# Performance work log

Hardware: AMD Instinct MI355X
Metric: run time of the kernel (lower is better)

## Reference

```python
import jax, jax.numpy as jnp
import numpy as np

TAU = 0.5

def setup_inputs() -> dict:
    key = jax.random.key(0)
    ks = jax.random.split(key, 8)
    B_Nq, B_Ns, C, H, W = 16, 16, 512, 32, 32
    f_q = jax.random.normal(ks[0], (B_Nq, C, H, W), dtype=jnp.float32)
    f_s = jax.random.normal(ks[1], (B_Ns, C, H, W), dtype=jnp.float32)
    # depthwise 1x1 convs with groups=dim, bias=False -> per-channel scalar weights [C]
    w_cca_q = jax.random.normal(ks[2], (C,), dtype=jnp.float32)
    w_cca_k = jax.random.normal(ks[3], (C,), dtype=jnp.float32)
    w_cca_v = jax.random.normal(ks[4], (C,), dtype=jnp.float32)
    w_sca_q = jax.random.normal(ks[5], (C,), dtype=jnp.float32)
    w_sca_k = jax.random.normal(ks[6], (C,), dtype=jnp.float32)
    lam = jnp.float32(0.1)
    return {"f_q": f_q, "f_s": f_s, "w_cca_q": w_cca_q, "w_cca_k": w_cca_k,
            "w_cca_v": w_cca_v, "w_sca_q": w_sca_q, "w_sca_k": w_sca_k, "lam": lam}

def _dw(x, w):
    # depthwise 1x1 conv, no bias == per-channel scale; x: [B,C,H,W], w: [C]
    return x * w[None, :, None, None]

def reference(f_q, f_s, w_cca_q, w_cca_k, w_cca_v, w_sca_q, w_sca_k, lam):
    B_Nq, C, H, W = f_q.shape
    B_Ns = f_s.shape[0]
    P = H * W
    qc = _dw(f_q, w_cca_q).reshape(B_Nq, C, P)          # [B,C,P]
    kc_mean = _dw(f_s, w_cca_k).reshape(B_Ns, C, P).mean(axis=0)  # [C,P]
    vc_mean = _dw(f_s, w_cca_v).reshape(B_Ns, C, P).mean(axis=0)  # [C,P]
    # channel attention: [B,C,C]
    Ac = jax.nn.softmax(jnp.einsum('bcp,dp->bcd', qc, kc_mean) / P, axis=-1)
    f_cca_q = jnp.einsum('bcd,dp->bcp', Ac, vc_mean).reshape(B_Nq, C, H, W)
    qs = _dw(f_cca_q, w_sca_q).reshape(B_Nq, C, P)      # [B,C,P]
    ks_mean = _dw(f_s, w_sca_k).reshape(B_Ns, C, P).mean(axis=0)  # [C,P]
    # spatial affinity: [B,P,P]
    M = jnp.einsum('bcp,cq->bpq', qs, ks_mean) / (TAU * C)
    alpha = jax.nn.softmax(M.mean(axis=-1), axis=-1)    # [B_Nq,P]
    beta = jax.nn.softmax(M.mean(axis=-2), axis=-1)     # [B_Nq,P]
    beta_mean = jnp.broadcast_to(beta.mean(axis=0, keepdims=True), (B_Ns, P))
    Fq_out = f_q + lam * f_cca_q
    return (Fq_out, alpha, beta_mean)
```

## Files before the change

kernel.cpp:

```cpp
#include <hip/hip_runtime.h>

typedef __bf16 bf16;
typedef __bf16 bf16x4 __attribute__((ext_vector_type(4)));
typedef __bf16 bf16x8 __attribute__((ext_vector_type(8)));
typedef float f32x4 __attribute__((ext_vector_type(4)));


#define GLL16(g, l)                                                             \
    __builtin_amdgcn_global_load_lds((const __attribute__((address_space(1))) void*)(g), \
                                     (__attribute__((address_space(3))) void*)(l), 16, 0, 0)

__device__ inline float wave_reduce_sum(float v) {
#pragma unroll
    for (int m = 32; m >= 1; m >>= 1) v += __shfl_xor(v, m, 64);
    return v;
}
__device__ inline float wave_reduce_max(float v) {
#pragma unroll
    for (int m = 32; m >= 1; m >>= 1) v = fmaxf(v, __shfl_xor(v, m, 64));
    return v;
}

__global__ void k_prep(const float* __restrict__ fs, const float* __restrict__ fq,
                       float* __restrict__ fsm32, bf16* __restrict__ fsm16,
                       bf16* __restrict__ fsmT, bf16* __restrict__ fq16) {
    __shared__ bf16 tile[32][33];
    int bx = blockIdx.x, by = blockIdx.y;
    int p0 = bx * 32, c0 = by * 32;
    int t = threadIdx.x, tx = t & 31, ty = t >> 5;
#pragma unroll
    for (int i = 0; i < 4; ++i) {
        size_t off = (size_t)(c0 + ty + 8 * i) * 1024 + p0 + tx;
        float s = 0.f;
#pragma unroll
        for (int b = 0; b < 16; ++b) s += fs[(size_t)b * 524288 + off];
        s *= (1.f / 16.f);
        fsm32[off] = s;
        bf16 h = (bf16)s;
        fsm16[off] = h;
        tile[ty + 8 * i][tx] = h;
    }
    __syncthreads();
#pragma unroll
    for (int i = 0; i < 4; ++i)
        fsmT[(size_t)(p0 + ty + 8 * i) * 512 + c0 + tx] = tile[tx][ty + 8 * i];
    int blk = by * 32 + bx;
    const float4* f4 = (const float4*)fq;
#pragma unroll
    for (int i = 0; i < 16; ++i) {
        int idx = blk * 4096 + i * 256 + t;
        float4 v = f4[idx];
        bf16x4 h4 = {(bf16)v.x, (bf16)v.y, (bf16)v.z, (bf16)v.w};
        *(bf16x4*)(fq16 + (size_t)idx * 4) = h4;
    }
}

__global__ void k_u(const float* __restrict__ fsm32, const float* __restrict__ wsq,
                    const float* __restrict__ wsk, float* __restrict__ u,
                    float* __restrict__ rm) {
    int c = blockIdx.x;
    int t = threadIdx.x;
    float s = 0.f;
#pragma unroll
    for (int j = 0; j < 4; ++j) s += fsm32[(size_t)c * 1024 + t + 256 * j];
    s = wave_reduce_sum(s);
    __shared__ float red[4];
    int w = t >> 6, lane = t & 63;
    if (lane == 0) red[w] = s;
    __syncthreads();
    if (t == 0) {
        float rmv = (red[0] + red[1] + red[2] + red[3]) * (1.f / 1024.f);
        rm[c] = rmv;
        u[c] = wsq[c] * wsk[c] * rmv * (1.f / 256.f);
    }
}

__global__ void k_gemm1(const bf16* __restrict__ A, const bf16* __restrict__ B,
                        float* __restrict__ G) {
    __shared__ alignas(16) bf16 As[64 * 32];
    __shared__ alignas(16) bf16 Bs[128 * 32];
    const int dt = blockIdx.x, ct = blockIdx.y, b = blockIdx.z;
    const int t = threadIdx.x, w = t >> 6, lane = t & 63;
    const int quad = lane >> 4, r15 = lane & 15;
    const bf16* Abase = A + ((size_t)(b * 512 + ct * 64)) * 1024;
    const bf16* Bbase = B + ((size_t)(dt * 128)) * 1024;
    const int sr = t >> 2, sc = (t & 3) * 8;
    f32x4 acc[8] = {};
    for (int k0 = 0; k0 < 1024; k0 += 32) {
        GLL16(Abase + (size_t)sr * 1024 + k0 + sc, As + t * 8);
        GLL16(Bbase + (size_t)sr * 1024 + k0 + sc, Bs + t * 8);
        GLL16(Bbase + (size_t)(sr + 64) * 1024 + k0 + sc, Bs + (t + 256) * 8);
        __syncthreads();
        bf16x8 af = *(const bf16x8*)(As + (w * 16 + r15) * 32 + quad * 8);
#pragma unroll
        for (int j = 0; j < 8; ++j) {
            bf16x8 bfr = *(const bf16x8*)(Bs + (j * 16 + r15) * 32 + quad * 8);
            acc[j] = __builtin_amdgcn_mfma_f32_16x16x32_bf16(af, bfr, acc[j], 0, 0, 0);
        }
        __syncthreads();
    }
    float* g = G + ((size_t)(b * 512 + ct * 64 + w * 16 + quad * 4)) * 512 + dt * 128 + r15;
#pragma unroll
    for (int j = 0; j < 8; ++j)
#pragma unroll
        for (int ii = 0; ii < 4; ++ii)
            g[(size_t)ii * 512 + j * 16] = acc[j][ii];
}

__global__ void k_softmax_ac(const float* __restrict__ G, const float* __restrict__ wq,
                             const float* __restrict__ wk, const float* __restrict__ wv,
                             const float* __restrict__ rm, bf16* __restrict__ Acw,
                             float* __restrict__ r) {
    int row = blockIdx.x * 4 + (threadIdx.x >> 6);
    int lane = threadIdx.x & 63;
    int c = row & 511;
    const float* g = G + (size_t)row * 512;
    float sc = wq[c] * (1.f / 1024.f);
    float v[8];
    float mx = -3.4e38f;
#pragma unroll
    for (int j = 0; j < 8; ++j) {
        int d = lane + 64 * j;
        v[j] = g[d] * sc * wk[d];
        mx = fmaxf(mx, v[j]);
    }
    mx = wave_reduce_max(mx);
    float sum = 0.f;
#pragma unroll
    for (int j = 0; j < 8; ++j) {
        v[j] = __expf(v[j] - mx);
        sum += v[j];
    }
    sum = wave_reduce_sum(sum);
    float inv = 1.f / sum;
    bf16* o = Acw + (size_t)row * 512;
    float rsum = 0.f;
#pragma unroll
    for (int j = 0; j < 8; ++j) {
        int d = lane + 64 * j;
        float aw = v[j] * inv * wv[d];
        o[d] = (bf16)aw;
        rsum += aw * rm[d];
    }
    rsum = wave_reduce_sum(rsum);
    if (lane == 0) r[row] = rsum;
}

__global__ void k_t(const bf16* __restrict__ Acw, const float* __restrict__ u,
                    float* __restrict__ tbp) {
    int half = blockIdx.z, b = blockIdx.y;
    int d = blockIdx.x * 256 + threadIdx.x;
    const bf16* base = Acw + (size_t)b * 262144 + (size_t)half * 256 * 512 + d;
    const float* uu = u + half * 256;
    float s = 0.f;
#pragma unroll 16
    for (int c = 0; c < 256; ++c) s += uu[c] * (float)base[(size_t)c * 512];
    tbp[(half * 16 + b) * 512 + d] = s;
}

__global__ void k_gemm2(const bf16* __restrict__ A, const bf16* __restrict__ B,
                        const float* __restrict__ fq, const float* __restrict__ lamp,
                        float* __restrict__ out) {
    __shared__ alignas(16) bf16 As[64 * 32];
    __shared__ alignas(16) bf16 Bs[128 * 32];
    const int pt = blockIdx.x, ct = blockIdx.y, b = blockIdx.z;
    const int t = threadIdx.x, w = t >> 6, lane = t & 63;
    const int quad = lane >> 4, r15 = lane & 15;
    const bf16* Abase = A + ((size_t)(b * 512 + ct * 64)) * 512;
    const bf16* Bbase = B + ((size_t)(pt * 128)) * 512;
    const int sr = t >> 2, sc = (t & 3) * 8;
    f32x4 acc[8] = {};
    for (int k0 = 0; k0 < 512; k0 += 32) {
        GLL16(Abase + (size_t)sr * 512 + k0 + sc, As + t * 8);
        GLL16(Bbase + (size_t)sr * 512 + k0 + sc, Bs + t * 8);
        GLL16(Bbase + (size_t)(sr + 64) * 512 + k0 + sc, Bs + (t + 256) * 8);
        __syncthreads();
        bf16x8 af = *(const bf16x8*)(As + (w * 16 + r15) * 32 + quad * 8);
#pragma unroll
        for (int j = 0; j < 8; ++j) {
            bf16x8 bfr = *(const bf16x8*)(Bs + (j * 16 + r15) * 32 + quad * 8);
            acc[j] = __builtin_amdgcn_mfma_f32_16x16x32_bf16(af, bfr, acc[j], 0, 0, 0);
        }
        __syncthreads();
    }
    float lam = lamp[0];
    size_t rowbase = (size_t)(b * 512 + ct * 64 + w * 16 + quad * 4);
#pragma unroll
    for (int j = 0; j < 8; ++j)
#pragma unroll
        for (int ii = 0; ii < 4; ++ii) {
            size_t idx = (rowbase + ii) * 1024 + pt * 128 + j * 16 + r15;
            out[idx] = fq[idx] + lam * acc[j][ii];
        }
}

__global__ void k_logits(const float* __restrict__ tbp, const float* __restrict__ r,
                         const float* __restrict__ wsq, const float* __restrict__ wsk,
                         const float* __restrict__ fsm32, float* __restrict__ alog,
                         float* __restrict__ blog) {
    int z = blockIdx.y, pq = blockIdx.x * 256 + threadIdx.x;
    if (z < 16) {
        const float* t0 = tbp + z * 512;
        const float* t1 = tbp + (16 + z) * 512;
        float s = 0.f;
#pragma unroll 8
        for (int d = 0; d < 512; ++d) s += (t0[d] + t1[d]) * fsm32[(size_t)d * 1024 + pq];
        alog[z * 1024 + pq] = s;
    } else {
        int b = z - 16;
        float s = 0.f;
#pragma unroll 8
        for (int c = 0; c < 512; ++c) {
            float coef = r[b * 512 + c] * wsq[c] * wsk[c] * (1.f / 256.f);
            s += coef * fsm32[(size_t)c * 1024 + pq];
        }
        blog[b * 1024 + pq] = s;
    }
}

__global__ void k_softmax_rows(const float* __restrict__ alog, const float* __restrict__ blog,
                               float* __restrict__ alpha_out, float* __restrict__ beta) {
    int z = blockIdx.x;
    int t = threadIdx.x;
    int w = t >> 6, lane = t & 63;
    const float* src = (z < 16) ? (alog + (size_t)z * 1024) : (blog + (size_t)(z - 16) * 1024);
    float v[4];
    float mx = -3.4e38f;
#pragma unroll
    for (int j = 0; j < 4; ++j) {
        v[j] = src[t + 256 * j];
        mx = fmaxf(mx, v[j]);
    }
    __shared__ float red[4];
    float wm = wave_reduce_max(mx);
    if (lane == 0) red[w] = wm;
    __syncthreads();
    mx = fmaxf(fmaxf(red[0], red[1]), fmaxf(red[2], red[3]));
    float s = 0.f;
#pragma unroll
    for (int j = 0; j < 4; ++j) {
        v[j] = __expf(v[j] - mx);
        s += v[j];
    }
    __syncthreads();
    float ws_ = wave_reduce_sum(s);
    if (lane == 0) red[w] = ws_;
    __syncthreads();
    s = red[0] + red[1] + red[2] + red[3];
    float inv = 1.f / s;
    if (z < 16) {
#pragma unroll
        for (int j = 0; j < 4; ++j) alpha_out[(size_t)z * 1024 + t + 256 * j] = v[j] * inv;
    } else {
#pragma unroll
        for (int j = 0; j < 4; ++j) beta[(size_t)(z - 16) * 1024 + t + 256 * j] = v[j] * inv;
    }
}

__global__ void k_betamean(const float* __restrict__ beta, float* __restrict__ out) {
    int q = blockIdx.x * 256 + threadIdx.x;
    float s = 0.f;
#pragma unroll
    for (int b = 0; b < 16; ++b) s += beta[b * 1024 + q];
    float val = s * (1.f / 16.f);
#pragma unroll
    for (int si = 0; si < 16; ++si) out[(size_t)si * 1024 + q] = val;
}

extern "C" void kernel_launch(void* const* d_in, const int* in_sizes, int n_in,
                              void* d_out, int out_size, void* d_ws, size_t ws_size,
                              hipStream_t stream) {
    const float* f_q = (const float*)d_in[0];
    const float* f_s = (const float*)d_in[1];
    const float* w_cca_q = (const float*)d_in[2];
    const float* w_cca_k = (const float*)d_in[3];
    const float* w_cca_v = (const float*)d_in[4];
    const float* w_sca_q = (const float*)d_in[5];
    const float* w_sca_k = (const float*)d_in[6];
    const float* lamp = (const float*)d_in[7];

    char* ws = (char*)d_ws;
    float* fsm32 = (float*)(ws + 0);
    bf16* fsm16 = (bf16*)(ws + 2097152);
    bf16* fsmT = (bf16*)(ws + 3145728);
    float* G = (float*)(ws + 4194304);
    bf16* Acw = (bf16*)(ws + 20971520);
    bf16* fq16 = (bf16*)(ws + 29360128);
    float* rm = (float*)(ws + 46137344);
    float* u = (float*)(ws + 46139392);
    float* r = (float*)(ws + 46141440);
    float* tbp = (float*)(ws + 46174208);
    float* alog = (float*)(ws + 46239744);
    float* blog = (float*)(ws + 46305280);
    float* beta = (float*)(ws + 46370816);

    float* out_fq = (float*)d_out;
    float* out_alpha = out_fq + 8388608;
    float* out_bmean = out_fq + 8404992;

    k_prep<<<dim3(32, 16), 256, 0, stream>>>(f_s, f_q, fsm32, fsm16, fsmT, fq16);
    k_u<<<512, 256, 0, stream>>>(fsm32, w_sca_q, w_sca_k, u, rm);
    k_gemm1<<<dim3(4, 8, 16), 256, 0, stream>>>(fq16, fsm16, G);
    k_softmax_ac<<<2048, 256, 0, stream>>>(G, w_cca_q, w_cca_k, w_cca_v, rm, Acw, r);
    k_t<<<dim3(2, 16, 2), 256, 0, stream>>>(Acw, u, tbp);
    k_gemm2<<<dim3(8, 8, 16), 256, 0, stream>>>(Acw, fsmT, f_q, lamp, out_fq);
    k_logits<<<dim3(4, 32), 256, 0, stream>>>(tbp, r, w_sca_q, w_sca_k, fsm32, alog, blog);
    k_softmax_rows<<<32, 256, 0, stream>>>(alog, blog, out_alpha, beta);
    k_betamean<<<4, 256, 0, stream>>>(beta, out_bmean);
}
```

Before: 204.6 us.

## Fuse row-mean into prep via atomics, merge logits with softmax, drop k_u

Computes the per-channel spatial sum inside k_prep with wave shuffles and atomicAdd, which removes the separate k_u launch. A memset is added so the accumulator starts at zero. k_t now builds its u coefficients itself and splits the channels into four chunks for more blocks. The logits and row-softmax kernels become one 1024-thread kernel, which drops the intermediate alog/blog buffers and a launch. The trade-offs are atomic contention, an extra memset call, and fewer blocks (32) doing the logits dot products.

```diff
diff --git a/kernel.cpp b/kernel.cpp
--- a/kernel.cpp
+++ b/kernel.cpp
@@ -23,11 +23,13 @@
 
 __global__ void k_prep(const float* __restrict__ fs, const float* __restrict__ fq,
                        float* __restrict__ fsm32, bf16* __restrict__ fsm16,
-                       bf16* __restrict__ fsmT, bf16* __restrict__ fq16) {
+                       bf16* __restrict__ fsmT, bf16* __restrict__ fq16,
+                       float* __restrict__ rm) {
     __shared__ bf16 tile[32][33];
     int bx = blockIdx.x, by = blockIdx.y;
     int p0 = bx * 32, c0 = by * 32;
     int t = threadIdx.x, tx = t & 31, ty = t >> 5;
+    float rs[4];
 #pragma unroll
     for (int i = 0; i < 4; ++i) {
         size_t off = (size_t)(c0 + ty + 8 * i) * 1024 + p0 + tx;
@@ -39,6 +41,14 @@
         bf16 h = (bf16)s;
         fsm16[off] = h;
         tile[ty + 8 * i][tx] = h;
+        rs[i] = s;
+    }
+#pragma unroll
+    for (int i = 0; i < 4; ++i) {
+        float v = rs[i];
+#pragma unroll
+        for (int m = 16; m >= 1; m >>= 1) v += __shfl_xor(v, m, 64);
+        if (tx == 0) atomicAdd(&rm[c0 + ty + 8 * i], v);
     }
     __syncthreads();
 #pragma unroll
@@ -52,26 +62,6 @@
         float4 v = f4[idx];
         bf16x4 h4 = {(bf16)v.x, (bf16)v.y, (bf16)v.z, (bf16)v.w};
         *(bf16x4*)(fq16 + (size_t)idx * 4) = h4;
-    }
-}
-
-__global__ void k_u(const float* __restrict__ fsm32, const float* __restrict__ wsq,
-                    const float* __restrict__ wsk, float* __restrict__ u,
-                    float* __restrict__ rm) {
-    int c = blockIdx.x;
-    int t = threadIdx.x;
-    float s = 0.f;
-#pragma unroll
-    for (int j = 0; j < 4; ++j) s += fsm32[(size_t)c * 1024 + t + 256 * j];
-    s = wave_reduce_sum(s);
-    __shared__ float red[4];
-    int w = t >> 6, lane = t & 63;
-    if (lane == 0) red[w] = s;
-    __syncthreads();
-    if (t == 0) {
-        float rmv = (red[0] + red[1] + red[2] + red[3]) * (1.f / 1024.f);
-        rm[c] = rmv;
-        u[c] = wsq[c] * wsk[c] * rmv * (1.f / 256.f);
     }
 }
 
@@ -140,22 +130,10 @@
         int d = lane + 64 * j;
         float aw = v[j] * inv * wv[d];
         o[d] = (bf16)aw;
-        rsum += aw * rm[d];
+        rsum += aw * rm[d] * (1.f / 1024.f);
     }
     rsum = wave_reduce_sum(rsum);
     if (lane == 0) r[row] = rsum;
-}
-
-__global__ void k_t(const bf16* __restrict__ Acw, const float* __restrict__ u,
-                    float* __restrict__ tbp) {
-    int half = blockIdx.z, b = blockIdx.y;
-    int d = blockIdx.x * 256 + threadIdx.x;
-    const bf16* base = Acw + (size_t)b * 262144 + (size_t)half * 256 * 512 + d;
-    const float* uu = u + half * 256;
-    float s = 0.f;
-#pragma unroll 16
-    for (int c = 0; c < 256; ++c) s += uu[c] * (float)base[(size_t)c * 512];
-    tbp[(half * 16 + b) * 512 + d] = s;
 }
 
 __global__ void k_gemm2(const bf16* __restrict__ A, const bf16* __restrict__ B,
@@ -194,67 +172,62 @@
         }
 }
 
-__global__ void k_logits(const float* __restrict__ tbp, const float* __restrict__ r,
-                         const float* __restrict__ wsq, const float* __restrict__ wsk,
-                         const float* __restrict__ fsm32, float* __restrict__ alog,
-                         float* __restrict__ blog) {
-    int z = blockIdx.y, pq = blockIdx.x * 256 + threadIdx.x;
-    if (z < 16) {
-        const float* t0 = tbp + z * 512;
-        const float* t1 = tbp + (16 + z) * 512;
-        float s = 0.f;
+__global__ void k_t(const bf16* __restrict__ Acw, const float* __restrict__ rm,
+                    const float* __restrict__ wsq, const float* __restrict__ wsk,
+                    float* __restrict__ tbp) {
+    __shared__ float u_sh[128];
+    int q = blockIdx.z, b = blockIdx.y;
+    int d = blockIdx.x * 256 + threadIdx.x;
+    if (threadIdx.x < 128) {
+        int c = q * 128 + threadIdx.x;
+        u_sh[threadIdx.x] = rm[c] * wsq[c] * wsk[c] * (1.f / 262144.f);
+    }
+    __syncthreads();
+    const bf16* base = Acw + (size_t)b * 262144 + (size_t)q * 128 * 512 + d;
+    float s = 0.f;
+#pragma unroll 16
+    for (int c = 0; c < 128; ++c) s += u_sh[c] * (float)base[(size_t)c * 512];
+    tbp[(q * 16 + b) * 512 + d] = s;
+}
+
+__global__ __launch_bounds__(1024) void k_logsoft(
+    const float* __restrict__ tbp, const float* __restrict__ r,
+    const float* __restrict__ wsq, const float* __restrict__ wsk,
+    const float* __restrict__ fsm32, float* __restrict__ alpha_out,
+    float* __restrict__ beta) {
+    __shared__ float coef[512];
+    __shared__ float red[16];
+    int z = blockIdx.x, t = threadIdx.x, w = t >> 6, lane = t & 63;
+    if (t < 512) {
+        if (z < 16)
+            coef[t] = tbp[z * 512 + t] + tbp[(16 + z) * 512 + t] +
+                      tbp[(32 + z) * 512 + t] + tbp[(48 + z) * 512 + t];
+        else
+            coef[t] = r[(z - 16) * 512 + t] * wsq[t] * wsk[t] * (1.f / 256.f);
+    }
+    __syncthreads();
+    float s = 0.f;
 #pragma unroll 8
-        for (int d = 0; d < 512; ++d) s += (t0[d] + t1[d]) * fsm32[(size_t)d * 1024 + pq];
-        alog[z * 1024 + pq] = s;
-    } else {
-        int b = z - 16;
-        float s = 0.f;
-#pragma unroll 8
-        for (int c = 0; c < 512; ++c) {
-            float coef = r[b * 512 + c] * wsq[c] * wsk[c] * (1.f / 256.f);
-            s += coef * fsm32[(size_t)c * 1024 + pq];
-        }
-        blog[b * 1024 + pq] = s;
-    }
-}
-
-__global__ void k_softmax_rows(const float* __restrict__ alog, const float* __restrict__ blog,
-                               float* __restrict__ alpha_out, float* __restrict__ beta) {
-    int z = blockIdx.x;
-    int t = threadIdx.x;
-    int w = t >> 6, lane = t & 63;
-    const float* src = (z < 16) ? (alog + (size_t)z * 1024) : (blog + (size_t)(z - 16) * 1024);
-    float v[4];
-    float mx = -3.4e38f;
-#pragma unroll
-    for (int j = 0; j < 4; ++j) {
-        v[j] = src[t + 256 * j];
-        mx = fmaxf(mx, v[j]);
-    }
-    __shared__ float red[4];
-    float wm = wave_reduce_max(mx);
-    if (lane == 0) red[w] = wm;
-    __syncthreads();
-    mx = fmaxf(fmaxf(red[0], red[1]), fmaxf(red[2], red[3]));
-    float s = 0.f;
-#pragma unroll
-    for (int j = 0; j < 4; ++j) {
-        v[j] = __expf(v[j] - mx);
-        s += v[j];
-    }
-    __syncthreads();
-    float ws_ = wave_reduce_sum(s);
-    if (lane == 0) red[w] = ws_;
-    __syncthreads();
-    s = red[0] + red[1] + red[2] + red[3];
-    float inv = 1.f / s;
-    if (z < 16) {
-#pragma unroll
-        for (int j = 0; j < 4; ++j) alpha_out[(size_t)z * 1024 + t + 256 * j] = v[j] * inv;
-    } else {
-#pragma unroll
-        for (int j = 0; j < 4; ++j) beta[(size_t)(z - 16) * 1024 + t + 256 * j] = v[j] * inv;
-    }
+    for (int d = 0; d < 512; ++d) s = fmaf(coef[d], fsm32[(size_t)d * 1024 + t], s);
+    float mx = s;
+#pragma unroll
+    for (int m = 32; m >= 1; m >>= 1) mx = fmaxf(mx, __shfl_xor(mx, m, 64));
+    if (lane == 0) red[w] = mx;
+    __syncthreads();
+    float m2 = red[0];
+#pragma unroll
+    for (int i = 1; i < 16; ++i) m2 = fmaxf(m2, red[i]);
+    __syncthreads();
+    float e = __expf(s - m2);
+    float ss = wave_reduce_sum(e);
+    if (lane == 0) red[w] = ss;
+    __syncthreads();
+    float tot = 0.f;
+#pragma unroll
+    for (int i = 0; i < 16; ++i) tot += red[i];
+    float val = e / tot;
+    if (z < 16) alpha_out[(size_t)z * 1024 + t] = val;
+    else beta[(size_t)(z - 16) * 1024 + t] = val;
 }
 
 __global__ void k_betamean(const float* __restrict__ beta, float* __restrict__ out) {
@@ -283,28 +256,24 @@
     float* fsm32 = (float*)(ws + 0);
     bf16* fsm16 = (bf16*)(ws + 2097152);
     bf16* fsmT = (bf16*)(ws + 3145728);
-    float* G = (float*)(ws + 4194304);
-    bf16* Acw = (bf16*)(ws + 20971520);
-    bf16* fq16 = (bf16*)(ws + 29360128);
+    bf16* fq16 = (bf16*)(ws + 4194304);
+    float* G = (float*)(ws + 20971520);
+    bf16* Acw = (bf16*)(ws + 37748736);
     float* rm = (float*)(ws + 46137344);
-    float* u = (float*)(ws + 46139392);
-    float* r = (float*)(ws + 46141440);
-    float* tbp = (float*)(ws + 46174208);
-    float* alog = (float*)(ws + 46239744);
-    float* blog = (float*)(ws + 46305280);
-    float* beta = (float*)(ws + 46370816);
+    float* tbp = (float*)(ws + 46139392);
+    float* r = (float*)(ws + 46270464);
+    float* beta = (float*)(ws + 46303232);
 
     float* out_fq = (float*)d_out;
     float* out_alpha = out_fq + 8388608;
     float* out_bmean = out_fq + 8404992;
 
-    k_prep<<<dim3(32, 16), 256, 0, stream>>>(f_s, f_q, fsm32, fsm16, fsmT, fq16);
-    k_u<<<512, 256, 0, stream>>>(fsm32, w_sca_q, w_sca_k, u, rm);
+    hipMemsetAsync(ws + 46137344, 0, 133120, stream);
+    k_prep<<<dim3(32, 16), 256, 0, stream>>>(f_s, f_q, fsm32, fsm16, fsmT, fq16, rm);
     k_gemm1<<<dim3(4, 8, 16), 256, 0, stream>>>(fq16, fsm16, G);
     k_softmax_ac<<<2048, 256, 0, stream>>>(G, w_cca_q, w_cca_k, w_cca_v, rm, Acw, r);
-    k_t<<<dim3(2, 16, 2), 256, 0, stream>>>(Acw, u, tbp);
     k_gemm2<<<dim3(8, 8, 16), 256, 0, stream>>>(Acw, fsmT, f_q, lamp, out_fq);
-    k_logits<<<dim3(4, 32), 256, 0, stream>>>(tbp, r, w_sca_q, w_sca_k, fsm32, alog, blog);
-    k_softmax_rows<<<32, 256, 0, stream>>>(alog, blog, out_alpha, beta);
+    k_t<<<dim3(2, 16, 4), 256, 0, stream>>>(Acw, rm, w_sca_q, w_sca_k, tbp);
+    k_logsoft<<<32, 1024, 0, stream>>>(tbp, r, w_sca_q, w_sca_k, fsm32, out_alpha, beta);
     k_betamean<<<4, 256, 0, stream>>>(beta, out_bmean);
 }
```

Measured after the change: 207.4 us. About the same (+1.3%).
